# Kernel tuning notes

Measured on AMD Instinct MI355X. Metric: run time of the kernel, lower is better.

## Reference

```python
import jax, jax.numpy as jnp
import numpy as np

N, E, F_IN, H, O = 50000, 800000, 128, 64, 1


def _gcn_conv(x, row, col, ew, W, b, n_nodes):
    """PyG GCNConv: add self-loops (weight 1), symmetric deg normalization,
    linear transform (no bias inside lin), scatter-add aggregation, then +bias."""
    loop = jnp.arange(n_nodes, dtype=row.dtype)
    r = jnp.concatenate([row, loop])
    c = jnp.concatenate([col, loop])
    w = jnp.concatenate([ew, jnp.ones((n_nodes,), dtype=ew.dtype)])
    deg = jax.ops.segment_sum(w, c, num_segments=n_nodes)            # [N]
    dis = jnp.where(deg > 0, jax.lax.rsqrt(jnp.maximum(deg, 1e-12)), 0.0)
    norm = dis[r] * w * dis[c]                                       # [E+N]
    h = x @ W                                                        # [N, out]
    msg = h[r] * norm[:, None]                                       # gather + scale
    agg = jax.ops.segment_sum(msg, c, num_segments=n_nodes)          # scatter-add
    return agg + b


def setup_inputs() -> dict:
    key = jax.random.key(0)
    ks = jax.random.split(key, 14)
    s = 0.02
    return {
        "x": jax.random.normal(ks[0], (N, F_IN), dtype=jnp.float32),
        "edge_index": jax.random.randint(ks[1], (2, E), 0, N, dtype=jnp.int64),
        "edge_weight": jax.random.uniform(ks[2], (E,), dtype=jnp.float32),
        "W1": jax.random.normal(ks[3], (F_IN, H), dtype=jnp.float32) * s,
        "b1": jnp.zeros((H,), dtype=jnp.float32),
        "W2": jax.random.normal(ks[4], (H, H), dtype=jnp.float32) * s,
        "b2": jnp.zeros((H,), dtype=jnp.float32),
        "W_ih": jax.random.normal(ks[5], (4 * H, H), dtype=jnp.float32) * s,
        "W_hh": jax.random.normal(ks[6], (4 * H, H), dtype=jnp.float32) * s,
        "b_ih": jax.random.normal(ks[7], (4 * H,), dtype=jnp.float32) * s,
        "b_hh": jax.random.normal(ks[8], (4 * H,), dtype=jnp.float32) * s,
        "W_reg": jax.random.normal(ks[9], (H, O), dtype=jnp.float32) * s,
        "b_reg": jnp.zeros((O,), dtype=jnp.float32),
    }


def reference(x, edge_index, edge_weight, W1, b1, W2, b2,
              W_ih, W_hh, b_ih, b_hh, W_reg, b_reg):
    row, col = edge_index[0], edge_index[1]
    n = x.shape[0]
    h = jax.nn.relu(_gcn_conv(x, row, col, edge_weight, W1, b1, n))
    h = jax.nn.relu(_gcn_conv(h, row, col, edge_weight, W2, b2, n))
    # single-step LSTM, zero initial (h0, c0); PyTorch gate order i, f, g, o
    hd = W_ih.shape[1]
    h0 = jnp.zeros((n, hd), dtype=h.dtype)
    gates = h @ W_ih.T + h0 @ W_hh.T + b_ih + b_hh                   # [N, 4H]
    i, f, g, o = jnp.split(gates, 4, axis=-1)
    c = jax.nn.sigmoid(f) * 0.0 + jax.nn.sigmoid(i) * jnp.tanh(g)    # c0 = 0
    hn = jax.nn.sigmoid(o) * jnp.tanh(c)                             # lstm_out[:, -1]
    return hn @ W_reg + b_reg
```

## Files before the change

### kernel.cpp

```cpp
#include <hip/hip_runtime.h>
#include <math.h>


#define QN 6272
#define NOCT 8
#define NPAD (NOCT * QN)
#define NSLICE 128

__device__ __forceinline__ float sigmoidf_(float x) {
    return 1.0f / (1.0f + expf(-x));
}

__global__ __launch_bounds__(256) void hist_k(const int* __restrict__ col,
                                              unsigned short* __restrict__ part,
                                              int E, int N) {
    __shared__ int hc[QN];
    const int t = threadIdx.x;
    const int s = blockIdx.x >> 3;
    const int q = blockIdx.x & 7;
    const int lo = q * QN;
    for (int i = t; i < QN; i += 256) hc[i] = 0;
    __syncthreads();
    const int per = (E + NSLICE - 1) / NSLICE;
    const int e0 = s * per, e1 = min(E, e0 + per);
    int e = e0 + t;
    for (; e + 768 < e1; e += 1024) {
        int c0 = col[e], c1 = col[e + 256], c2 = col[e + 512], c3 = col[e + 768];
        unsigned r0 = (unsigned)(c0 - lo), r1 = (unsigned)(c1 - lo);
        unsigned r2 = (unsigned)(c2 - lo), r3 = (unsigned)(c3 - lo);
        if (r0 < (unsigned)QN && (unsigned)c0 < (unsigned)N) atomicAdd(&hc[r0], 1);
        if (r1 < (unsigned)QN && (unsigned)c1 < (unsigned)N) atomicAdd(&hc[r1], 1);
        if (r2 < (unsigned)QN && (unsigned)c2 < (unsigned)N) atomicAdd(&hc[r2], 1);
        if (r3 < (unsigned)QN && (unsigned)c3 < (unsigned)N) atomicAdd(&hc[r3], 1);
    }
    for (; e < e1; e += 256) {
        int c = col[e];
        unsigned rel = (unsigned)(c - lo);
        if (rel < (unsigned)QN && (unsigned)c < (unsigned)N) atomicAdd(&hc[rel], 1);
    }
    __syncthreads();
    unsigned short* dst = part + (size_t)s * NPAD + lo;
    for (int i = t; i < QN; i += 256) dst[i] = (unsigned short)hc[i];
}

__global__ __launch_bounds__(256) void prefix_k(const unsigned short* __restrict__ part,
                                                unsigned short* __restrict__ coff,
                                                int* __restrict__ cnt) {
    int i = blockIdx.x * 256 + threadIdx.x;
    int acc = 0;
    for (int s = 0; s < NSLICE; ++s) {
        size_t idx = (size_t)s * NPAD + i;
        coff[idx] = (unsigned short)acc;
        acc += part[idx];
    }
    cnt[i] = acc;
}

__global__ __launch_bounds__(256) void scanA_k(const int* __restrict__ cnt,
                                               int* __restrict__ bsum, int N) {
    __shared__ int r[256];
    int t = threadIdx.x, i = blockIdx.x * 256 + t;
    r[t] = (i < N) ? cnt[i] : 0;
    __syncthreads();
#pragma unroll
    for (int off = 128; off > 0; off >>= 1) {
        if (t < off) r[t] += r[t + off];
        __syncthreads();
    }
    if (t == 0) bsum[blockIdx.x] = r[0];
}

__global__ __launch_bounds__(256) void scanB_k(int* __restrict__ bsum,
                                               int* __restrict__ rowptr, int NB, int N) {
    __shared__ int s[2][256];
    int t = threadIdx.x;
    int v = (t < NB) ? bsum[t] : 0;
    int pin = 0;
    s[0][t] = v;
    __syncthreads();
#pragma unroll
    for (int off = 1; off < 256; off <<= 1) {
        int x = s[pin][t];
        if (t >= off) x += s[pin][t - off];
        s[pin ^ 1][t] = x;
        pin ^= 1;
        __syncthreads();
    }
    int incl = s[pin][t];
    if (t < NB) bsum[t] = incl - v;
    if (t == 255) rowptr[N] = incl;
}

__global__ __launch_bounds__(256) void scanC_k(const int* __restrict__ cnt,
                                               const int* __restrict__ bsum,
                                               int* __restrict__ rowptr, int N) {
    __shared__ int s[2][256];
    int t = threadIdx.x, i = blockIdx.x * 256 + t;
    int v = (i < N) ? cnt[i] : 0;
    int pin = 0;
    s[0][t] = v;
    __syncthreads();
#pragma unroll
    for (int off = 1; off < 256; off <<= 1) {
        int x = s[pin][t];
        if (t >= off) x += s[pin][t - off];
        s[pin ^ 1][t] = x;
        pin ^= 1;
        __syncthreads();
    }
    int excl = s[pin][t] - v + bsum[blockIdx.x];
    if (i < N) rowptr[i] = excl;
}

__global__ __launch_bounds__(256) void fill_k(const int* __restrict__ row,
                                              const int* __restrict__ col,
                                              const float* __restrict__ ew,
                                              const int* __restrict__ rowptr,
                                              const unsigned short* __restrict__ coff,
                                              int2* __restrict__ pairs, int E, int N) {
    __shared__ int lcur[QN];
    const int t = threadIdx.x;
    const int s = blockIdx.x >> 3;
    const int q = blockIdx.x & 7;
    const int lo = q * QN;
    const unsigned short* cof = coff + (size_t)s * NPAD + lo;
    const int* rp = rowptr + lo;
    for (int i = t; i < QN; i += 256) lcur[i] = rp[i] + (int)cof[i];
    __syncthreads();
    const int per = (E + NSLICE - 1) / NSLICE;
    const int e0 = s * per, e1 = min(E, e0 + per);
    int e = e0 + t;
    for (; e + 768 < e1; e += 1024) {
        int c0 = col[e], c1 = col[e + 256], c2 = col[e + 512], c3 = col[e + 768];
        unsigned r0 = (unsigned)(c0 - lo), r1 = (unsigned)(c1 - lo);
        unsigned r2 = (unsigned)(c2 - lo), r3 = (unsigned)(c3 - lo);
        if (r0 < (unsigned)QN && (unsigned)c0 < (unsigned)N) {
            int r = row[e]; float w = ew[e];
            if ((unsigned)r >= (unsigned)N) { r = 0; w = 0.0f; }
            pairs[atomicAdd(&lcur[r0], 1)] = make_int2(r, __float_as_int(w));
        }
        if (r1 < (unsigned)QN && (unsigned)c1 < (unsigned)N) {
            int r = row[e + 256]; float w = ew[e + 256];
            if ((unsigned)r >= (unsigned)N) { r = 0; w = 0.0f; }
            pairs[atomicAdd(&lcur[r1], 1)] = make_int2(r, __float_as_int(w));
        }
        if (r2 < (unsigned)QN && (unsigned)c2 < (unsigned)N) {
            int r = row[e + 512]; float w = ew[e + 512];
            if ((unsigned)r >= (unsigned)N) { r = 0; w = 0.0f; }
            pairs[atomicAdd(&lcur[r2], 1)] = make_int2(r, __float_as_int(w));
        }
        if (r3 < (unsigned)QN && (unsigned)c3 < (unsigned)N) {
            int r = row[e + 768]; float w = ew[e + 768];
            if ((unsigned)r >= (unsigned)N) { r = 0; w = 0.0f; }
            pairs[atomicAdd(&lcur[r3], 1)] = make_int2(r, __float_as_int(w));
        }
    }
    for (; e < e1; e += 256) {
        int c = col[e];
        unsigned rel = (unsigned)(c - lo);
        if (rel < (unsigned)QN && (unsigned)c < (unsigned)N) {
            int r = row[e]; float w = ew[e];
            if ((unsigned)r >= (unsigned)N) { r = 0; w = 0.0f; }
            pairs[atomicAdd(&lcur[rel], 1)] = make_int2(r, __float_as_int(w));
        }
    }
}

__global__ __launch_bounds__(256) void degsum_k(const int* __restrict__ rowptr,
                                                const int2* __restrict__ pairs,
                                                float* __restrict__ dis, int N) {
    int i = blockIdx.x * 256 + threadIdx.x;
    if (i >= N) return;
    int b = rowptr[i], en = rowptr[i + 1];
    float s = 0.0f;
    for (int e = b; e < en; ++e) s += __int_as_float(pairs[e].y);
    dis[i] = rsqrtf(s + 1.0f);
}

__global__ __launch_bounds__(256) void scale_k(int2* __restrict__ pairs,
                                               const float* __restrict__ dis, int E) {
    int e = blockIdx.x * 256 + threadIdx.x;
    if (e >= E) return;
    int2 p = pairs[e];
    p.y = __float_as_int(__int_as_float(p.y) * dis[p.x]);
    pairs[e] = p;
}

__global__ __launch_bounds__(256) void aggregate_k(const float* __restrict__ h,
                                                   const int* __restrict__ rowptr,
                                                   const int2* __restrict__ pairs,
                                                   const float* __restrict__ dis,
                                                   const float* __restrict__ b,
                                                   float* __restrict__ out, int N) {
    const int t = threadIdx.x;
    const int lane = t & 63;
    const int n0 = (blockIdx.x * 4 + (t >> 6)) * 2;
    if (n0 >= N) return;
    const int n1 = n0 + 1;

    const int beg0 = rowptr[n0];
    const int end0 = rowptr[n0 + 1];
    const int beg1 = end0;
    const int end1 = (n1 < N) ? rowptr[n1 + 1] : end0;
    const int len0 = end0 - beg0, len1 = end1 - beg1;
    const int L = max(len0, len1);

    float acc0 = 0.0f, acc1 = 0.0f;
    for (int base = 0; base < L; base += 64) {
        const int m0 = min(64, len0 - base);
        const int m1 = min(64, len1 - base);
        int s0r = 0, s1r = 0; float v0r = 0.0f, v1r = 0.0f;
        if (lane < m0) {
            int2 p = pairs[beg0 + base + lane];
            s0r = p.x; v0r = __int_as_float(p.y);
        }
        if (lane < m1) {
            int2 p = pairs[beg1 + base + lane];
            s1r = p.x; v1r = __int_as_float(p.y);
        }
        const int m = max(m0, m1);
        int j = 0;
        for (; j + 4 <= m; j += 4) {
            int   a0 = __shfl(s0r, j),     a1 = __shfl(s0r, j + 1);
            int   a2 = __shfl(s0r, j + 2), a3 = __shfl(s0r, j + 3);
            int   b0 = __shfl(s1r, j),     b1 = __shfl(s1r, j + 1);
            int   b2 = __shfl(s1r, j + 2), b3 = __shfl(s1r, j + 3);
            float x0 = __shfl(v0r, j),     x1 = __shfl(v0r, j + 1);
            float x2 = __shfl(v0r, j + 2), x3 = __shfl(v0r, j + 3);
            float y0 = __shfl(v1r, j),     y1 = __shfl(v1r, j + 1);
            float y2 = __shfl(v1r, j + 2), y3 = __shfl(v1r, j + 3);
            float ha0 = h[(size_t)a0 * 64 + lane];
            float ha1 = h[(size_t)a1 * 64 + lane];
            float ha2 = h[(size_t)a2 * 64 + lane];
            float ha3 = h[(size_t)a3 * 64 + lane];
            float hb0 = h[(size_t)b0 * 64 + lane];
            float hb1 = h[(size_t)b1 * 64 + lane];
            float hb2 = h[(size_t)b2 * 64 + lane];
            float hb3 = h[(size_t)b3 * 64 + lane];
            acc0 = fmaf(ha0, x0, acc0); acc0 = fmaf(ha1, x1, acc0);
            acc0 = fmaf(ha2, x2, acc0); acc0 = fmaf(ha3, x3, acc0);
            acc1 = fmaf(hb0, y0, acc1); acc1 = fmaf(hb1, y1, acc1);
            acc1 = fmaf(hb2, y2, acc1); acc1 = fmaf(hb3, y3, acc1);
        }
        for (; j < m; ++j) {
            int   a0 = __shfl(s0r, j), b0 = __shfl(s1r, j);
            float x0 = __shfl(v0r, j), y0 = __shfl(v1r, j);
            acc0 = fmaf(h[(size_t)a0 * 64 + lane], x0, acc0);
            acc1 = fmaf(h[(size_t)b0 * 64 + lane], y0, acc1);
        }
    }
    {
        float d = dis[n0];
        acc0 = fmaf(d, h[(size_t)n0 * 64 + lane], acc0);
        acc0 = fmaf(d, acc0, b[lane]);
        out[(size_t)n0 * 64 + lane] = fmaxf(acc0, 0.0f);
    }
    if (n1 < N) {
        float d = dis[n1];
        acc1 = fmaf(d, h[(size_t)n1 * 64 + lane], acc1);
        acc1 = fmaf(d, acc1, b[lane]);
        out[(size_t)n1 * 64 + lane] = fmaxf(acc1, 0.0f);
    }
}

template <int K>
__global__ __launch_bounds__(256) void gemm64_k(const float* __restrict__ A,
                                                const float* __restrict__ W,
                                                float* __restrict__ C, int M) {
    __shared__ float xs[64][68];
    __shared__ float ws[K][64];
    const int t  = threadIdx.x;
    const int n0 = blockIdx.x * 64;

    for (int base = t * 4; base < K * 64; base += 1024)
        *(float4*)((float*)ws + base) = *(const float4*)(W + base);

    const int cg = t & 15, ng = t >> 4;
    const int col = cg * 4, nb = ng * 4;
    float acc[4][4];
#pragma unroll
    for (int i = 0; i < 4; ++i)
#pragma unroll
        for (int j = 0; j < 4; ++j) acc[i][j] = 0.0f;

    for (int k0 = 0; k0 < K; k0 += 64) {
        __syncthreads();
        for (int base = t * 4; base < 64 * 64; base += 1024) {
            int r = base >> 6, k = base & 63;
            int node = n0 + r;
            float4 v = make_float4(0.f, 0.f, 0.f, 0.f);
            if (node < M) v = *(const float4*)(A + (size_t)node * K + k0 + k);
            *(float4*)&xs[r][k] = v;
        }
        __syncthreads();
#pragma unroll 4
        for (int kk = 0; kk < 64; kk += 4) {
            float4 a[4];
#pragma unroll
            for (int i = 0; i < 4; ++i) a[i] = *(float4*)&xs[nb + i][kk];
#pragma unroll
            for (int j = 0; j < 4; ++j) {
                float4 bv = *(float4*)&ws[k0 + kk + j][col];
                float av[4];
                switch (j) {
                    case 0: av[0]=a[0].x; av[1]=a[1].x; av[2]=a[2].x; av[3]=a[3].x; break;
                    case 1: av[0]=a[0].y; av[1]=a[1].y; av[2]=a[2].y; av[3]=a[3].y; break;
                    case 2: av[0]=a[0].z; av[1]=a[1].z; av[2]=a[2].z; av[3]=a[3].z; break;
                    default:av[0]=a[0].w; av[1]=a[1].w; av[2]=a[2].w; av[3]=a[3].w; break;
                }
#pragma unroll
                for (int i = 0; i < 4; ++i) {
                    acc[i][0] = fmaf(av[i], bv.x, acc[i][0]);
                    acc[i][1] = fmaf(av[i], bv.y, acc[i][1]);
                    acc[i][2] = fmaf(av[i], bv.z, acc[i][2]);
                    acc[i][3] = fmaf(av[i], bv.w, acc[i][3]);
                }
            }
        }
    }
#pragma unroll
    for (int i = 0; i < 4; ++i) {
        int node = n0 + nb + i;
        if (node < M)
            *(float4*)(C + (size_t)node * 64 + col) =
                make_float4(acc[i][0], acc[i][1], acc[i][2], acc[i][3]);
    }
}

__global__ __launch_bounds__(256) void lstm_head_k(const float* __restrict__ h,
                                                   const float* __restrict__ Wih,
                                                   const float* __restrict__ bih,
                                                   const float* __restrict__ bhh,
                                                   const float* __restrict__ Wreg,
                                                   const float* __restrict__ breg,
                                                   float* __restrict__ out, int N) {
    __shared__ float wt[64 * 192];
    __shared__ float hsT[64 * 64];
    const int t = threadIdx.x;
    const int n0 = blockIdx.x * 64;

    {
        const int j = t & 63, kq = (t >> 6) * 4;
#pragma unroll
        for (int gid = 0; gid < 3; ++gid) {
            const int gBase = (gid == 0) ? 0 : (gid == 1 ? 128 : 192);
            const int gOff = gid * 64;
#pragma unroll
            for (int it = 0; it < 4; ++it) {
                int k0 = it * 16 + kq;
                float4 w = *(const float4*)(Wih + (size_t)(gBase + j) * 64 + k0);
                wt[(k0 + 0) * 192 + gOff + j] = w.x;
                wt[(k0 + 1) * 192 + gOff + j] = w.y;
                wt[(k0 + 2) * 192 + gOff + j] = w.z;
                wt[(k0 + 3) * 192 + gOff + j] = w.w;
            }
        }
    }
    {
        const int r = t & 63, kq = (t >> 6) * 4;
        const int node = n0 + r;
#pragma unroll
        for (int it = 0; it < 4; ++it) {
            int k0 = it * 16 + kq;
            float4 v = make_float4(0.f, 0.f, 0.f, 0.f);
            if (node < N) v = *(const float4*)(h + (size_t)node * 64 + k0);
            hsT[(k0 + 0) * 64 + r] = v.x;
            hsT[(k0 + 1) * 64 + r] = v.y;
            hsT[(k0 + 2) * 64 + r] = v.z;
            hsT[(k0 + 3) * 64 + r] = v.w;
        }
    }

    const int cg = t & 15, ng = t >> 4;
    const int col = cg * 4, nb = ng * 4;
    float4 bi4 = *(const float4*)(bih + col);
    float4 bg4 = *(const float4*)(bih + 128 + col);
    float4 bo4 = *(const float4*)(bih + 192 + col);
    {
        float4 h0 = *(const float4*)(bhh + col);
        float4 h1 = *(const float4*)(bhh + 128 + col);
        float4 h2 = *(const float4*)(bhh + 192 + col);
        bi4.x += h0.x; bi4.y += h0.y; bi4.z += h0.z; bi4.w += h0.w;
        bg4.x += h1.x; bg4.y += h1.y; bg4.z += h1.z; bg4.w += h1.w;
        bo4.x += h2.x; bo4.y += h2.y; bo4.z += h2.z; bo4.w += h2.w;
    }
    float4 wr4 = *(const float4*)(Wreg + col);
    const float br = breg[0];

    __syncthreads();

    float ai[4][4], ag[4][4], ao[4][4];
#pragma unroll
    for (int i = 0; i < 4; ++i)
#pragma unroll
        for (int j = 0; j < 4; ++j) { ai[i][j] = 0.f; ag[i][j] = 0.f; ao[i][j] = 0.f; }

#pragma unroll 4
    for (int k = 0; k < 64; ++k) {
        float4 a  = *(float4*)&hsT[k * 64 + nb];
        float4 wi = *(float4*)&wt[k * 192 + col];
        float4 wg = *(float4*)&wt[k * 192 + 64 + col];
        float4 wo = *(float4*)&wt[k * 192 + 128 + col];
        const float av[4] = {a.x, a.y, a.z, a.w};
#pragma unroll
        for (int i = 0; i < 4; ++i) {
            ai[i][0] = fmaf(av[i], wi.x, ai[i][0]);
            ai[i][1] = fmaf(av[i], wi.y, ai[i][1]);
            ai[i][2] = fmaf(av[i], wi.z, ai[i][2]);
            ai[i][3] = fmaf(av[i], wi.w, ai[i][3]);
            ag[i][0] = fmaf(av[i], wg.x, ag[i][0]);
            ag[i][1] = fmaf(av[i], wg.y, ag[i][1]);
            ag[i][2] = fmaf(av[i], wg.z, ag[i][2]);
            ag[i][3] = fmaf(av[i], wg.w, ag[i][3]);
            ao[i][0] = fmaf(av[i], wo.x, ao[i][0]);
            ao[i][1] = fmaf(av[i], wo.y, ao[i][1]);
            ao[i][2] = fmaf(av[i], wo.z, ao[i][2]);
            ao[i][3] = fmaf(av[i], wo.w, ao[i][3]);
        }
    }

    const float bia[4] = {bi4.x, bi4.y, bi4.z, bi4.w};
    const float bga[4] = {bg4.x, bg4.y, bg4.z, bg4.w};
    const float boa[4] = {bo4.x, bo4.y, bo4.z, bo4.w};
    const float wra[4] = {wr4.x, wr4.y, wr4.z, wr4.w};
    float res[4];
#pragma unroll
    for (int i = 0; i < 4; ++i) {
        float s = 0.f;
#pragma unroll
        for (int j = 0; j < 4; ++j) {
            float gi = ai[i][j] + bia[j];
            float gg = ag[i][j] + bga[j];
            float go = ao[i][j] + boa[j];
            float cc = sigmoidf_(gi) * tanhf(gg);
            float hn = sigmoidf_(go) * tanhf(cc);
            s = fmaf(hn, wra[j], s);
        }
        res[i] = s;
    }
#pragma unroll
    for (int off = 8; off > 0; off >>= 1) {
#pragma unroll
        for (int i = 0; i < 4; ++i) res[i] += __shfl_down(res[i], off);
    }
    if (cg == 0) {
#pragma unroll
        for (int i = 0; i < 4; ++i) {
            int node = n0 + nb + i;
            if (node < N) out[node] = res[i] + br;
        }
    }
}

extern "C" void kernel_launch(void* const* d_in, const int* in_sizes, int n_in,
                              void* d_out, int out_size, void* d_ws, size_t ws_size,
                              hipStream_t stream) {
    const float* x    = (const float*)d_in[0];
    const int*   ei   = (const int*)d_in[1];
    const float* ew   = (const float*)d_in[2];
    const float* W1   = (const float*)d_in[3];
    const float* b1   = (const float*)d_in[4];
    const float* W2   = (const float*)d_in[5];
    const float* b2   = (const float*)d_in[6];
    const float* Wih  = (const float*)d_in[7];
    const float* bih  = (const float*)d_in[9];
    const float* bhh  = (const float*)d_in[10];
    const float* Wreg = (const float*)d_in[11];
    const float* breg = (const float*)d_in[12];
    float* out = (float*)d_out;

    const int N = out_size;
    const int E = in_sizes[1] / 2;
    const int* row = ei;
    const int* col = ei + E;

    const int NB = (N + 255) / 256;
    const int eb = (E + 255) / 256;

    const size_t R16 = (size_t)NSLICE * NPAD * 2;
    const size_t RF  = (size_t)N * 64 * 4;
    const size_t REG = (R16 > RF ? R16 : RF + 255) & ~(size_t)255;

    char* wsb = (char*)d_ws;
    size_t off = 0;
    unsigned short* part = (unsigned short*)(wsb + off);
    float*          bufA = (float*)(wsb + off); off += REG;
    unsigned short* coff = (unsigned short*)(wsb + off);
    float*          bufC = (float*)(wsb + off); off += REG;
    float*          bufB = (float*)(wsb + off); off += REG;
    int2*  pairs  = (int2*) (wsb + off); off += (size_t)E * 8;
    float* dis    = (float*)(wsb + off); off += (size_t)NPAD * 4;
    int*   cnt    = (int*)  (wsb + off); off += (size_t)NPAD * 4;
    int*   rowptr = (int*)  (wsb + off); off += ((size_t)NPAD + 64) * 4;
    int*   bsum   = (int*)  (wsb + off); off += 1024;

    const int gb = (N + 63) / 64;
    const int ab = (N + 7) / 8;

    hist_k<<<NSLICE * NOCT, 256, 0, stream>>>(col, part, E, N);
    prefix_k<<<NPAD / 256, 256, 0, stream>>>(part, coff, cnt);
    scanA_k<<<NB, 256, 0, stream>>>(cnt, bsum, N);
    scanB_k<<<1, 256, 0, stream>>>(bsum, rowptr, NB, N);
    scanC_k<<<NB, 256, 0, stream>>>(cnt, bsum, rowptr, N);
    fill_k<<<NSLICE * NOCT, 256, 0, stream>>>(row, col, ew, rowptr, coff, pairs, E, N);
    degsum_k<<<NB, 256, 0, stream>>>(rowptr, pairs, dis, N);
    scale_k<<<eb, 256, 0, stream>>>(pairs, dis, E);

    gemm64_k<128><<<gb, 256, 0, stream>>>(x, W1, bufA, N);
    aggregate_k<<<ab, 256, 0, stream>>>(bufA, rowptr, pairs, dis, b1, bufB, N);

    gemm64_k<64><<<gb, 256, 0, stream>>>(bufB, W2, bufC, N);
    aggregate_k<<<ab, 256, 0, stream>>>(bufC, rowptr, pairs, dis, b2, bufA, N);

    lstm_head_k<<<gb, 256, 0, stream>>>(bufA, Wih, bih, bhh, Wreg, breg, out, N);
}
```

Before: 280.3 us.

## Fuse histogram with first GEMM, merge scan kernels, fold edge scaling into aggregation

```diff
diff --git a/kernel.cpp b/kernel.cpp
--- a/kernel.cpp
+++ b/kernel.cpp
@@ -6,47 +6,111 @@
 #define NOCT 8
 #define NPAD (NOCT * QN)
 #define NSLICE 128
+#define HIST_BLOCKS (NSLICE * NOCT)
 
 __device__ __forceinline__ float sigmoidf_(float x) {
     return 1.0f / (1.0f + expf(-x));
 }
 
-__global__ __launch_bounds__(256) void hist_k(const int* __restrict__ col,
-                                              unsigned short* __restrict__ part,
-                                              int E, int N) {
-    __shared__ int hc[QN];
+__global__ __launch_bounds__(256) void hist_gemm1_k(
+        const int* __restrict__ col, unsigned short* __restrict__ part,
+        int E, int N,
+        const float* __restrict__ x, const float* __restrict__ W1,
+        float* __restrict__ C) {
+    extern __shared__ char smem[];
     const int t = threadIdx.x;
-    const int s = blockIdx.x >> 3;
-    const int q = blockIdx.x & 7;
-    const int lo = q * QN;
-    for (int i = t; i < QN; i += 256) hc[i] = 0;
-    __syncthreads();
-    const int per = (E + NSLICE - 1) / NSLICE;
-    const int e0 = s * per, e1 = min(E, e0 + per);
-    int e = e0 + t;
-    for (; e + 768 < e1; e += 1024) {
-        int c0 = col[e], c1 = col[e + 256], c2 = col[e + 512], c3 = col[e + 768];
-        unsigned r0 = (unsigned)(c0 - lo), r1 = (unsigned)(c1 - lo);
-        unsigned r2 = (unsigned)(c2 - lo), r3 = (unsigned)(c3 - lo);
-        if (r0 < (unsigned)QN && (unsigned)c0 < (unsigned)N) atomicAdd(&hc[r0], 1);
-        if (r1 < (unsigned)QN && (unsigned)c1 < (unsigned)N) atomicAdd(&hc[r1], 1);
-        if (r2 < (unsigned)QN && (unsigned)c2 < (unsigned)N) atomicAdd(&hc[r2], 1);
-        if (r3 < (unsigned)QN && (unsigned)c3 < (unsigned)N) atomicAdd(&hc[r3], 1);
-    }
-    for (; e < e1; e += 256) {
-        int c = col[e];
-        unsigned rel = (unsigned)(c - lo);
-        if (rel < (unsigned)QN && (unsigned)c < (unsigned)N) atomicAdd(&hc[rel], 1);
-    }
-    __syncthreads();
-    unsigned short* dst = part + (size_t)s * NPAD + lo;
-    for (int i = t; i < QN; i += 256) dst[i] = (unsigned short)hc[i];
-}
-
-__global__ __launch_bounds__(256) void prefix_k(const unsigned short* __restrict__ part,
-                                                unsigned short* __restrict__ coff,
-                                                int* __restrict__ cnt) {
-    int i = blockIdx.x * 256 + threadIdx.x;
+    if (blockIdx.x < HIST_BLOCKS) {
+        int* hc = (int*)smem;
+        const int s = blockIdx.x >> 3;
+        const int q = blockIdx.x & 7;
+        const int lo = q * QN;
+        for (int i = t; i < QN; i += 256) hc[i] = 0;
+        __syncthreads();
+        const int per = (E + NSLICE - 1) / NSLICE;
+        const int e0 = s * per, e1 = min(E, e0 + per);
+        int e = e0 + t;
+        for (; e + 768 < e1; e += 1024) {
+            int c0 = col[e], c1 = col[e + 256], c2 = col[e + 512], c3 = col[e + 768];
+            unsigned r0 = (unsigned)(c0 - lo), r1 = (unsigned)(c1 - lo);
+            unsigned r2 = (unsigned)(c2 - lo), r3 = (unsigned)(c3 - lo);
+            if (r0 < (unsigned)QN && (unsigned)c0 < (unsigned)N) atomicAdd(&hc[r0], 1);
+            if (r1 < (unsigned)QN && (unsigned)c1 < (unsigned)N) atomicAdd(&hc[r1], 1);
+            if (r2 < (unsigned)QN && (unsigned)c2 < (unsigned)N) atomicAdd(&hc[r2], 1);
+            if (r3 < (unsigned)QN && (unsigned)c3 < (unsigned)N) atomicAdd(&hc[r3], 1);
+        }
+        for (; e < e1; e += 256) {
+            int c = col[e];
+            unsigned rel = (unsigned)(c - lo);
+            if (rel < (unsigned)QN && (unsigned)c < (unsigned)N) atomicAdd(&hc[rel], 1);
+        }
+        __syncthreads();
+        unsigned short* dst = part + (size_t)s * NPAD + lo;
+        for (int i = t; i < QN; i += 256) dst[i] = (unsigned short)hc[i];
+    } else {
+        float (*xs)[68] = (float (*)[68])smem;
+        float* ws = (float*)(smem + 64 * 68 * sizeof(float));
+        const int n0 = (int)(blockIdx.x - HIST_BLOCKS) * 64;
+        for (int base = t * 4; base < 128 * 64; base += 1024)
+            *(float4*)(ws + base) = *(const float4*)(W1 + base);
+        const int cg = t & 15, ng = t >> 4;
+        const int colj = cg * 4, nb = ng * 4;
+        float acc[4][4];
+#pragma unroll
+        for (int i = 0; i < 4; ++i)
+#pragma unroll
+            for (int j = 0; j < 4; ++j) acc[i][j] = 0.0f;
+        for (int k0 = 0; k0 < 128; k0 += 64) {
+            __syncthreads();
+            for (int base = t * 4; base < 64 * 64; base += 1024) {
+                int r = base >> 6, k = base & 63;
+                int node = n0 + r;
+                float4 v = make_float4(0.f, 0.f, 0.f, 0.f);
+                if (node < N) v = *(const float4*)(x + (size_t)node * 128 + k0 + k);
+                *(float4*)&xs[r][k] = v;
+            }
+            __syncthreads();
+#pragma unroll 4
+            for (int kk = 0; kk < 64; kk += 4) {
+                float4 a[4];
+#pragma unroll
+                for (int i = 0; i < 4; ++i) a[i] = *(float4*)&xs[nb + i][kk];
+#pragma unroll
+                for (int j = 0; j < 4; ++j) {
+                    float4 bv = *(float4*)&ws[(size_t)(k0 + kk + j) * 64 + colj];
+                    float av[4];
+                    switch (j) {
+                        case 0: av[0]=a[0].x; av[1]=a[1].x; av[2]=a[2].x; av[3]=a[3].x; break;
+                        case 1: av[0]=a[0].y; av[1]=a[1].y; av[2]=a[2].y; av[3]=a[3].y; break;
+                        case 2: av[0]=a[0].z; av[1]=a[1].z; av[2]=a[2].z; av[3]=a[3].z; break;
+                        default:av[0]=a[0].w; av[1]=a[1].w; av[2]=a[2].w; av[3]=a[3].w; break;
+                    }
+#pragma unroll
+                    for (int i = 0; i < 4; ++i) {
+                        acc[i][0] = fmaf(av[i], bv.x, acc[i][0]);
+                        acc[i][1] = fmaf(av[i], bv.y, acc[i][1]);
+                        acc[i][2] = fmaf(av[i], bv.z, acc[i][2]);
+                        acc[i][3] = fmaf(av[i], bv.w, acc[i][3]);
+                    }
+                }
+            }
+        }
+#pragma unroll
+        for (int i = 0; i < 4; ++i) {
+            int node = n0 + nb + i;
+            if (node < N)
+                *(float4*)(C + (size_t)node * 64 + colj) =
+                    make_float4(acc[i][0], acc[i][1], acc[i][2], acc[i][3]);
+        }
+    }
+}
+
+__global__ __launch_bounds__(256) void prefixA_k(const unsigned short* __restrict__ part,
+                                                 unsigned short* __restrict__ coff,
+                                                 int* __restrict__ cnt,
+                                                 int* __restrict__ bsum) {
+    __shared__ int r[256];
+    const int t = threadIdx.x;
+    const int i = blockIdx.x * 256 + t;
     int acc = 0;
     for (int s = 0; s < NSLICE; ++s) {
         size_t idx = (size_t)s * NPAD + i;
@@ -54,13 +118,7 @@
         acc += part[idx];
     }
     cnt[i] = acc;
-}
-
-__global__ __launch_bounds__(256) void scanA_k(const int* __restrict__ cnt,
-                                               int* __restrict__ bsum, int N) {
-    __shared__ int r[256];
-    int t = threadIdx.x, i = blockIdx.x * 256 + t;
-    r[t] = (i < N) ? cnt[i] : 0;
+    r[t] = acc;
     __syncthreads();
 #pragma unroll
     for (int off = 128; off > 0; off >>= 1) {
@@ -70,46 +128,34 @@
     if (t == 0) bsum[blockIdx.x] = r[0];
 }
 
-__global__ __launch_bounds__(256) void scanB_k(int* __restrict__ bsum,
-                                               int* __restrict__ rowptr, int NB, int N) {
+__global__ __launch_bounds__(256) void scanBC_k(const int* __restrict__ cnt,
+                                                const int* __restrict__ bsum,
+                                                int* __restrict__ rowptr, int NBLK) {
     __shared__ int s[2][256];
-    int t = threadIdx.x;
-    int v = (t < NB) ? bsum[t] : 0;
+    __shared__ int red[256];
+    const int t = threadIdx.x, b = blockIdx.x;
+    const int i = b * 256 + t;
+    int v = cnt[i];
     int pin = 0;
     s[0][t] = v;
     __syncthreads();
 #pragma unroll
     for (int off = 1; off < 256; off <<= 1) {
-        int x = s[pin][t];
-        if (t >= off) x += s[pin][t - off];
-        s[pin ^ 1][t] = x;
+        int xo = s[pin][t];
+        if (t >= off) xo += s[pin][t - off];
+        s[pin ^ 1][t] = xo;
         pin ^= 1;
         __syncthreads();
     }
-    int incl = s[pin][t];
-    if (t < NB) bsum[t] = incl - v;
-    if (t == 255) rowptr[N] = incl;
-}
-
-__global__ __launch_bounds__(256) void scanC_k(const int* __restrict__ cnt,
-                                               const int* __restrict__ bsum,
-                                               int* __restrict__ rowptr, int N) {
-    __shared__ int s[2][256];
-    int t = threadIdx.x, i = blockIdx.x * 256 + t;
-    int v = (i < N) ? cnt[i] : 0;
-    int pin = 0;
-    s[0][t] = v;
+    int excl = s[pin][t] - v;
+    red[t] = (t < b && t < NBLK) ? bsum[t] : 0;
     __syncthreads();
 #pragma unroll
-    for (int off = 1; off < 256; off <<= 1) {
-        int x = s[pin][t];
-        if (t >= off) x += s[pin][t - off];
-        s[pin ^ 1][t] = x;
-        pin ^= 1;
-        __syncthreads();
-    }
-    int excl = s[pin][t] - v + bsum[blockIdx.x];
-    if (i < N) rowptr[i] = excl;
+    for (int off = 128; off > 0; off >>= 1) {
+        if (t < off) red[t] += red[t + off];
+        __syncthreads();
+    }
+    rowptr[i] = excl + red[0];
 }
 
 __global__ __launch_bounds__(256) void fill_k(const int* __restrict__ row,
@@ -177,89 +223,77 @@
     dis[i] = rsqrtf(s + 1.0f);
 }
 
-__global__ __launch_bounds__(256) void scale_k(int2* __restrict__ pairs,
-                                               const float* __restrict__ dis, int E) {
-    int e = blockIdx.x * 256 + threadIdx.x;
-    if (e >= E) return;
-    int2 p = pairs[e];
-    p.y = __float_as_int(__int_as_float(p.y) * dis[p.x]);
-    pairs[e] = p;
-}
-
 __global__ __launch_bounds__(256) void aggregate_k(const float* __restrict__ h,
                                                    const int* __restrict__ rowptr,
                                                    const int2* __restrict__ pairs,
                                                    const float* __restrict__ dis,
-                                                   const float* __restrict__ b,
+                                                   const float* __restrict__ bias,
                                                    float* __restrict__ out, int N) {
+    __shared__ int2 pl[4][4][64];
     const int t = threadIdx.x;
-    const int lane = t & 63;
-    const int n0 = (blockIdx.x * 4 + (t >> 6)) * 2;
+    const int lane = t & 63, w = t >> 6;
+    const int n0 = (blockIdx.x * 4 + w) * 4;
     if (n0 >= N) return;
-    const int n1 = n0 + 1;
-
-    const int beg0 = rowptr[n0];
-    const int end0 = rowptr[n0 + 1];
-    const int beg1 = end0;
-    const int end1 = (n1 < N) ? rowptr[n1 + 1] : end0;
-    const int len0 = end0 - beg0, len1 = end1 - beg1;
-    const int L = max(len0, len1);
-
-    float acc0 = 0.0f, acc1 = 0.0f;
+
+    int rp[5];
+#pragma unroll
+    for (int k = 0; k < 5; ++k) rp[k] = rowptr[min(n0 + k, N)];
+    int len[4]; int L = 0;
+#pragma unroll
+    for (int i = 0; i < 4; ++i) { len[i] = rp[i + 1] - rp[i]; L = max(L, len[i]); }
+
+    float acc[4] = {0.f, 0.f, 0.f, 0.f};
     for (int base = 0; base < L; base += 64) {
-        const int m0 = min(64, len0 - base);
-        const int m1 = min(64, len1 - base);
-        int s0r = 0, s1r = 0; float v0r = 0.0f, v1r = 0.0f;
-        if (lane < m0) {
-            int2 p = pairs[beg0 + base + lane];
-            s0r = p.x; v0r = __int_as_float(p.y);
-        }
-        if (lane < m1) {
-            int2 p = pairs[beg1 + base + lane];
-            s1r = p.x; v1r = __int_as_float(p.y);
-        }
-        const int m = max(m0, m1);
+#pragma unroll
+        for (int i = 0; i < 4; ++i) {
+            int m = len[i] - base;
+            int2 p = make_int2(0, 0);
+            if (lane < m) {
+                p = pairs[rp[i] + base + lane];
+                p.y = __float_as_int(__int_as_float(p.y) * dis[p.x]);
+            }
+            pl[w][i][lane] = p;
+        }
+        const int m = min(64, L - base);
         int j = 0;
         for (; j + 4 <= m; j += 4) {
-            int   a0 = __shfl(s0r, j),     a1 = __shfl(s0r, j + 1);
-            int   a2 = __shfl(s0r, j + 2), a3 = __shfl(s0r, j + 3);
-            int   b0 = __shfl(s1r, j),     b1 = __shfl(s1r, j + 1);
-            int   b2 = __shfl(s1r, j + 2), b3 = __shfl(s1r, j + 3);
-            float x0 = __shfl(v0r, j),     x1 = __shfl(v0r, j + 1);
-            float x2 = __shfl(v0r, j + 2), x3 = __shfl(v0r, j + 3);
-            float y0 = __shfl(v1r, j),     y1 = __shfl(v1r, j + 1);
-            float y2 = __shfl(v1r, j + 2), y3 = __shfl(v1r, j + 3);
-            float ha0 = h[(size_t)a0 * 64 + lane];
-            float ha1 = h[(size_t)a1 * 64 + lane];
-            float ha2 = h[(size_t)a2 * 64 + lane];
-            float ha3 = h[(size_t)a3 * 64 + lane];
-            float hb0 = h[(size_t)b0 * 64 + lane];
-            float hb1 = h[(size_t)b1 * 64 + lane];
-            float hb2 = h[(size_t)b2 * 64 + lane];
-            float hb3 = h[(size_t)b3 * 64 + lane];
-            acc0 = fmaf(ha0, x0, acc0); acc0 = fmaf(ha1, x1, acc0);
-            acc0 = fmaf(ha2, x2, acc0); acc0 = fmaf(ha3, x3, acc0);
-            acc1 = fmaf(hb0, y0, acc1); acc1 = fmaf(hb1, y1, acc1);
-            acc1 = fmaf(hb2, y2, acc1); acc1 = fmaf(hb3, y3, acc1);
+#pragma unroll
+            for (int jj = 0; jj < 4; ++jj) {
+                int2 p0 = pl[w][0][j + jj];
+                int2 p1 = pl[w][1][j + jj];
+                int2 p2 = pl[w][2][j + jj];
+                int2 p3 = pl[w][3][j + jj];
+                float h0 = h[(size_t)p0.x * 64 + lane];
+                float h1 = h[(size_t)p1.x * 64 + lane];
+                float h2 = h[(size_t)p2.x * 64 + lane];
+                float h3 = h[(size_t)p3.x * 64 + lane];
+                acc[0] = fmaf(h0, __int_as_float(p0.y), acc[0]);
+                acc[1] = fmaf(h1, __int_as_float(p1.y), acc[1]);
+                acc[2] = fmaf(h2, __int_as_float(p2.y), acc[2]);
+                acc[3] = fmaf(h3, __int_as_float(p3.y), acc[3]);
+            }
         }
         for (; j < m; ++j) {
-            int   a0 = __shfl(s0r, j), b0 = __shfl(s1r, j);
-            float x0 = __shfl(v0r, j), y0 = __shfl(v1r, j);
-            acc0 = fmaf(h[(size_t)a0 * 64 + lane], x0, acc0);
-            acc1 = fmaf(h[(size_t)b0 * 64 + lane], y0, acc1);
-        }
-    }
-    {
-        float d = dis[n0];
-        acc0 = fmaf(d, h[(size_t)n0 * 64 + lane], acc0);
-        acc0 = fmaf(d, acc0, b[lane]);
-        out[(size_t)n0 * 64 + lane] = fmaxf(acc0, 0.0f);
-    }
-    if (n1 < N) {
-        float d = dis[n1];
-        acc1 = fmaf(d, h[(size_t)n1 * 64 + lane], acc1);
-        acc1 = fmaf(d, acc1, b[lane]);
-        out[(size_t)n1 * 64 + lane] = fmaxf(acc1, 0.0f);
+            int2 p0 = pl[w][0][j];
+            int2 p1 = pl[w][1][j];
+            int2 p2 = pl[w][2][j];
+            int2 p3 = pl[w][3][j];
+            acc[0] = fmaf(h[(size_t)p0.x * 64 + lane], __int_as_float(p0.y), acc[0]);
+            acc[1] = fmaf(h[(size_t)p1.x * 64 + lane], __int_as_float(p1.y), acc[1]);
+            acc[2] = fmaf(h[(size_t)p2.x * 64 + lane], __int_as_float(p2.y), acc[2]);
+            acc[3] = fmaf(h[(size_t)p3.x * 64 + lane], __int_as_float(p3.y), acc[3]);
+        }
+    }
+#pragma unroll
+    for (int i = 0; i < 4; ++i) {
+        int node = n0 + i;
+        if (node < N) {
+            float d = dis[node];
+            float a = acc[i];
+            a = fmaf(d, h[(size_t)node * 64 + lane], a);
+            a = fmaf(d, a, bias[lane]);
+            out[(size_t)node * 64 + lane] = fmaxf(a, 0.0f);
+        }
     }
 }
 
@@ -474,20 +508,16 @@
     const int* row = ei;
     const int* col = ei + E;
 
-    const int NB = (N + 255) / 256;
-    const int eb = (E + 255) / 256;
-
-    const size_t R16 = (size_t)NSLICE * NPAD * 2;
-    const size_t RF  = (size_t)N * 64 * 4;
-    const size_t REG = (R16 > RF ? R16 : RF + 255) & ~(size_t)255;
+    const int NB   = (N + 255) / 256;
+    const int NBLK = NPAD / 256;
 
     char* wsb = (char*)d_ws;
     size_t off = 0;
-    unsigned short* part = (unsigned short*)(wsb + off);
-    float*          bufA = (float*)(wsb + off); off += REG;
-    unsigned short* coff = (unsigned short*)(wsb + off);
-    float*          bufC = (float*)(wsb + off); off += REG;
-    float*          bufB = (float*)(wsb + off); off += REG;
+    unsigned short* part = (unsigned short*)(wsb + off); off += (size_t)NSLICE * NPAD * 2;
+    unsigned short* coff = (unsigned short*)(wsb + off); off += (size_t)NSLICE * NPAD * 2;
+    float* bufA   = (float*)(wsb + off); off += (size_t)N * 64 * 4;
+    float* bufB   = (float*)(wsb + off); off += (size_t)N * 64 * 4;
+    float* bufC   = (float*)(wsb + off); off += (size_t)N * 64 * 4;
     int2*  pairs  = (int2*) (wsb + off); off += (size_t)E * 8;
     float* dis    = (float*)(wsb + off); off += (size_t)NPAD * 4;
     int*   cnt    = (int*)  (wsb + off); off += (size_t)NPAD * 4;
@@ -495,22 +525,16 @@
     int*   bsum   = (int*)  (wsb + off); off += 1024;
 
     const int gb = (N + 63) / 64;
-    const int ab = (N + 7) / 8;
-
-    hist_k<<<NSLICE * NOCT, 256, 0, stream>>>(col, part, E, N);
-    prefix_k<<<NPAD / 256, 256, 0, stream>>>(part, coff, cnt);
-    scanA_k<<<NB, 256, 0, stream>>>(cnt, bsum, N);
-    scanB_k<<<1, 256, 0, stream>>>(bsum, rowptr, NB, N);
-    scanC_k<<<NB, 256, 0, stream>>>(cnt, bsum, rowptr, N);
-    fill_k<<<NSLICE * NOCT, 256, 0, stream>>>(row, col, ew, rowptr, coff, pairs, E, N);
+    const int ab = (N + 15) / 16;
+    const size_t DSM = 64 * 68 * sizeof(float) + 128 * 64 * sizeof(float);
+
+    hist_gemm1_k<<<HIST_BLOCKS + gb, 256, DSM, stream>>>(col, part, E, N, x, W1, bufA);
+    prefixA_k<<<NBLK, 256, 0, stream>>>(part, coff, cnt, bsum);
+    scanBC_k<<<NBLK, 256, 0, stream>>>(cnt, bsum, rowptr, NBLK);
+    fill_k<<<HIST_BLOCKS, 256, 0, stream>>>(row, col, ew, rowptr, coff, pairs, E, N);
     degsum_k<<<NB, 256, 0, stream>>>(rowptr, pairs, dis, N);
-    scale_k<<<eb, 256, 0, stream>>>(pairs, dis, E);
-
-    gemm64_k<128><<<gb, 256, 0, stream>>>(x, W1, bufA, N);
     aggregate_k<<<ab, 256, 0, stream>>>(bufA, rowptr, pairs, dis, b1, bufB, N);
-
     gemm64_k<64><<<gb, 256, 0, stream>>>(bufB, W2, bufC, N);
     aggregate_k<<<ab, 256, 0, stream>>>(bufC, rowptr, pairs, dis, b2, bufA, N);
-
     lstm_head_k<<<gb, 256, 0, stream>>>(bufA, Wih, bih, bhh, Wreg, breg, out, N);
 }
```

Result: no change. 280.9 us (+0.2%).
